# Performance work log

Hardware: AMD Instinct MI355X
Metric: run time of the kernel (lower is better)

## Reference

```python
import jax, jax.numpy as jnp
import numpy as np

B = 2048    # graphs in batch
V = 15      # nodes per graph
T = 16      # window (args.n_his)
F_IN = 2    # num_features
H = 64      # nhid
LH = 40     # LSTM hidden per direction
EPER = 40   # edges per graph
N = B * V
E = B * EPER
EPS = 1e-5


def setup_inputs() -> dict:
    key = jax.random.key(0)
    ks = jax.random.split(key, 12)

    def rn(k, shape, fan_in):
        return jax.random.normal(k, shape, jnp.float32) / np.sqrt(fan_in).astype(np.float32)

    # block-diagonal batched edge_index (PyG-style batching of B graphs of V nodes)
    rng = np.random.default_rng(0)
    off = np.arange(B)[:, None] * V
    src = rng.integers(0, V, (B, EPER)) + off
    dst = rng.integers(0, V, (B, EPER)) + off
    edge_index = jnp.asarray(np.stack([src.ravel(), dst.ravel()]), dtype=jnp.int32)

    return {
        "data": jax.random.normal(ks[0], (N, F_IN, T), jnp.float32),
        "edge_attr": jax.random.uniform(ks[1], (E,), jnp.float32),
        "W1": rn(ks[2], (H, F_IN), F_IN), "b1": jnp.zeros((H,), jnp.float32),
        "Wg1": rn(ks[3], (H, H), H), "bg1": jnp.zeros((H,), jnp.float32),
        "gamma1": jnp.ones((H,), jnp.float32), "beta1": jnp.zeros((H,), jnp.float32),
        "Wg2": rn(ks[4], (H, H), H), "bg2": jnp.zeros((H,), jnp.float32),
        "gamma2": jnp.ones((H,), jnp.float32), "beta2": jnp.zeros((H,), jnp.float32),
        "Wf": rn(ks[5], (H, V * H), V * H), "bf": jnp.zeros((H,), jnp.float32),
        "Wih_f": rn(ks[6], (4 * LH, H), H), "Whh_f": rn(ks[7], (4 * LH, LH), LH),
        "bih_f": jnp.zeros((4 * LH,), jnp.float32), "bhh_f": jnp.zeros((4 * LH,), jnp.float32),
        "Wih_b": rn(ks[8], (4 * LH, H), H), "Whh_b": rn(ks[9], (4 * LH, LH), LH),
        "bih_b": jnp.zeros((4 * LH,), jnp.float32), "bhh_b": jnp.zeros((4 * LH,), jnp.float32),
        "Wc1": rn(ks[10], (16, 2 * LH), 2 * LH), "bc1": jnp.zeros((16,), jnp.float32),
        "Wc2": rn(ks[11], (1, 16), 16), "bc2": jnp.zeros((1,), jnp.float32),
        "edge_index": edge_index,
    }


def _gcn(x, W, b, edge_index, ew):
    # PyG GCNConv: linear, add self-loops (weight 1), symmetric D^-1/2 (A+I) D^-1/2.
    # x: [N, T, H] -- all T timesteps processed at once (vectorizes the source loop).
    row, col = edge_index[0], edge_index[1]
    loop = jnp.arange(N, dtype=edge_index.dtype)
    row_s = jnp.concatenate([row, loop])
    col_s = jnp.concatenate([col, loop])
    ew_s = jnp.concatenate([ew, jnp.ones((N,), ew.dtype)])
    deg = jax.ops.segment_sum(ew_s, col_s, num_segments=N)
    dinv = jnp.where(deg > 0, jax.lax.rsqrt(deg), 0.0)
    norm = dinv[row_s] * ew_s * dinv[col_s]                      # [E+N]
    xw = jnp.einsum('nth,hk->ntk', x, W)                          # [N, T, H]
    agg = jax.ops.segment_sum(norm[:, None, None] * xw[row_s], col_s, num_segments=N)
    return agg + b


def _bn(x, gamma, beta):
    # BatchNorm1d training-mode stats, per timestep (axis 0 = nodes), biased var.
    m = x.mean(axis=0)
    v = x.var(axis=0)
    return gamma * (x - m) * jax.lax.rsqrt(v + EPS) + beta


def _lstm(X, Wih, Whh, bih, bhh):
    # X: [T, B, H]; PyTorch gate order i, f, g, o.
    def step(carry, xt):
        h, c = carry
        g = xt @ Wih.T + h @ Whh.T + (bih + bhh)
        i, f, gg, o = jnp.split(g, 4, axis=-1)
        c = jax.nn.sigmoid(f) * c + jax.nn.sigmoid(i) * jnp.tanh(gg)
        h = jax.nn.sigmoid(o) * jnp.tanh(c)
        return (h, c), h
    h0 = jnp.zeros((X.shape[1], LH), X.dtype)
    _, hs = jax.lax.scan(step, (h0, h0), X)
    return hs


def _forward(data, edge_attr, W1, b1, Wg1, bg1, gamma1, beta1, Wg2, bg2, gamma2, beta2,
             Wf, bf, Wih_f, Whh_f, bih_f, bhh_f, Wih_b, Whh_b, bih_b, bhh_b,
             Wc1, bc1, Wc2, bc2, edge_index):
    # conv_1 (1x1 Conv2d) == per-node linear over features, kept per timestep
    x = jnp.einsum('nft,hf->nth', data, W1) + b1                 # [N, T, H]
    # Hierarchical GCN with residuals (ReLU then BN, per the source)
    x1 = _bn(jax.nn.relu(_gcn(x, Wg1, bg1, edge_index, edge_attr)), gamma1, beta1) + x
    x2 = _bn(jax.nn.relu(_gcn(x1, Wg2, bg2, edge_index, edge_attr)), gamma2, beta2) + x1
    # stack over timesteps -> [T, B, V*H]
    Xs = x2.transpose(1, 0, 2).reshape(T, B, V * H)
    Xs = jax.nn.relu(Xs @ Wf.T + bf)                             # fc1 -> [T, B, H]
    hs_f = _lstm(Xs, Wih_f, Whh_f, bih_f, bhh_f)
    hs_b = _lstm(Xs[::-1], Wih_b, Whh_b, bih_b, bhh_b)
    # r_out[-1] = [fwd h at t=T-1, bwd h at t=T-1 (first step of reversed scan)]
    last = jnp.concatenate([hs_f[-1], hs_b[0]], axis=-1)          # [B, 80]
    hcls = jax.nn.relu(last @ Wc1.T + bc1)                        # dropout inactive (eval)
    return hcls @ Wc2.T + bc2                                     # [B, 1]


def reference(data, edge_attr, W1, b1, Wg1, bg1, gamma1, beta1, Wg2, bg2, gamma2, beta2,
              Wf, bf, Wih_f, Whh_f, bih_f, bhh_f, Wih_b, Whh_b, bih_b, bhh_b,
              Wc1, bc1, Wc2, bc2, edge_index):
    return _forward(data, edge_attr, W1, b1, Wg1, bg1, gamma1, beta1, Wg2, bg2,
                    gamma2, beta2, Wf, bf, Wih_f, Whh_f, bih_f, bhh_f,
                    Wih_b, Whh_b, bih_b, bhh_b, Wc1, bc1, Wc2, bc2, edge_index)
```

## Files before the change

### kernel.cpp

```cpp
#include <hip/hip_runtime.h>

typedef unsigned int u32;
typedef unsigned short u16;
typedef __attribute__((ext_vector_type(8))) short bf16x8;
typedef __attribute__((ext_vector_type(4))) float f32x4;

#define NB   2048
#define NV   15
#define NT   16
#define NH   64
#define NLH  40
#define EPER 40
#define NN   (NB*NV)
#define NE   (NB*EPER)

#define F_DATA 0
#define F_EA   983040
#define P_W1   1064960
#define P_B1   1065088
#define P_WG1  1065152
#define P_BG1  1069248
#define P_G1   1069312
#define P_BE1  1069376
#define P_WG2  1069440
#define P_BG2  1073536
#define P_G2   1073600
#define P_BE2  1073664
#define P_WF   1073728
#define P_BF   1135168
#define P_WIHF 1135232
#define P_WHHF 1145472
#define P_BIHF 1151872
#define P_BHHF 1152032
#define P_WIHB 1152192
#define P_WHHB 1162432
#define P_BIHB 1168832
#define P_BHHB 1168992
#define P_WC1  1169152
#define P_BC1  1170432
#define P_WC2  1170448
#define P_BC2  1170464
#define CVT_TOTAL 1170465
#define WFB_OFF   1170496
#define WIHT_OFF  1205504
#define STATS_OFF 1231936
#define XS_OFF    1240128
#define FLAG_OFF  3337280
#define BUFX_BYTE 13349376
#define BUFY_BYTE 76263936

__device__ const int d_cum[27] = {
  0, 983040, 1064960, 1065088, 1065152, 1069248, 1069312, 1069376,
  1069440, 1073536, 1073600, 1073664, 1073728, 1135168, 1135232, 1145472,
  1151872, 1152032, 1152192, 1162432, 1168832, 1168992, 1169152, 1170432,
  1170448, 1170464, 1170465};

struct Ptrs { const void* p[26]; };

__device__ inline float b2f(u16 u) { return __uint_as_float(((u32)u) << 16); }
__device__ inline u16 f2b(float f) {
  u32 u = __float_as_uint(f);
  u32 r = (u + 0x7FFFu + ((u >> 16) & 1u)) >> 16;
  return (u16)r;
}
__device__ inline float sigf(float x) { return 1.0f / (1.0f + __expf(-x)); }

__global__ void k_detect(const u16* __restrict__ raw, int* __restrict__ flag) {
  __shared__ int bad;
  if (threadIdx.x == 0) bad = 0;
  __syncthreads();
  for (int i = threadIdx.x; i < 4096; i += 256) {
    float f = b2f(raw[i]);
    if (!(fabsf(f) < 1000.0f)) atomicOr(&bad, 1);
  }
  __syncthreads();
  if (threadIdx.x == 0) *flag = bad ? 0 : 1;
}

__global__ void k_convert(Ptrs ptrs, float* __restrict__ W) {
  int gid = blockIdx.x * 256 + threadIdx.x;
  if (gid >= CVT_TOTAL) return;
  int flag = *(const int*)(W + FLAG_OFF);
  int ti = 0;
  #pragma unroll
  for (int i = 1; i < 26; ++i) ti += (gid >= d_cum[i]);
  int j = gid - d_cum[ti];
  const void* src = ptrs.p[ti];
  W[gid] = flag ? b2f(((const u16*)src)[j]) : ((const float*)src)[j];
}

__global__ void k_preswz(float* __restrict__ W, u16* __restrict__ WfB) {
  int i = blockIdx.x * 256 + threadIdx.x;
  if (i < 61440) {
    int j = i & 7, lane = (i >> 3) & 63, kt = (i >> 9) & 3, ks = i >> 11;
    int kout = kt * 16 + (lane & 15);
    int m = ks * 32 + ((lane >> 4) << 3) + j;
    WfB[i] = f2b(W[P_WF + kout * 960 + m]);
  } else if (i < 69632) {
    int ii = i - 61440;
    int L = ii >> 12, r = ii & 4095;
    int j = r & 7, lane = (r >> 3) & 63, nt = (r >> 9) & 3, ks = (r >> 11) & 1;
    int h = ks * 32 + ((lane >> 4) << 3) + j;
    int k = nt * 16 + (lane & 15);
    WfB[i] = f2b(W[(L ? P_WG2 : P_WG1) + h * 64 + k]);
  } else if (i < 90112) {
    int e = i - 69632;
    int which = e / 10240, rem = e % 10240;
    int kk = rem / 160, jj = rem % 160;
    W[WIHT_OFF + e] = W[(which ? P_WIHB : P_WIHF) + jj * 64 + kk];
  }
}

template<int LAYER>
__global__ __launch_bounds__(256, 4)
void k_gcn(const float* __restrict__ W, const int* __restrict__ ei,
           const u16* __restrict__ bufIn, u16* __restrict__ bufOut,
           const u16* __restrict__ WgB,
           float* __restrict__ S1, float* __restrict__ S2,
           int bgoff, int scoff, int shoff) {
  __shared__ u16 s_x[15360];
  __shared__ float s_m[240];
  __shared__ float s_deg[16];
  __shared__ float s_d[480];
  __shared__ float s_w1[192];

  int g = blockIdx.x, tid = threadIdx.x;
  float ew = 0.f; int er = 0, ec = 0;
  if (tid < 40) {
    er = ei[g * 40 + tid] - g * 15;
    ec = ei[NE + g * 40 + tid] - g * 15;
    ew = W[F_EA + g * 40 + tid];
  }
  if (tid >= 40 && tid < 56) s_deg[tid - 40] = 1.0f;
  for (int i = tid; i < 240; i += 256) s_m[i] = 0.f;
  if (tid >= 64 && tid < 184) ((float4*)s_d)[tid - 64] = ((const float4*)(W + F_DATA + g * 480))[tid - 64];
  if (tid >= 192 && tid < 240) ((float4*)s_w1)[tid - 192] = ((const float4*)(W + P_W1))[tid - 192];
  __syncthreads();

  if (tid < 40) atomicAdd(&s_deg[ec], ew);
  for (int i = tid; i < 1920; i += 256) {
    int v = i >> 7, rem = i & 127, t = rem >> 3, q = rem & 7;
    int h0 = q * 8;
    float d0 = s_d[v * 32 + t], d1 = s_d[v * 32 + 16 + t];
    u32 pk[4];
    if (LAYER == 1) {
      #pragma unroll
      for (int jp = 0; jp < 4; ++jp) {
        int h = h0 + jp * 2;
        float xa = fmaf(d0, s_w1[2 * h],     fmaf(d1, s_w1[2 * h + 1], s_w1[128 + h]));
        float xb = fmaf(d0, s_w1[2 * h + 2], fmaf(d1, s_w1[2 * h + 3], s_w1[129 + h]));
        pk[jp] = (u32)f2b(xa) | ((u32)f2b(xb) << 16);
      }
    } else {
      uint4 uy = ((const uint4*)(bufIn + g * 15360))[i];
      u32 uys[4] = {uy.x, uy.y, uy.z, uy.w};
      int th0 = t * 64 + h0;
      float4 A0 = *(const float4*)(W + scoff + th0), A1 = *(const float4*)(W + scoff + th0 + 4);
      float4 B0 = *(const float4*)(W + shoff + th0), B1 = *(const float4*)(W + shoff + th0 + 4);
      float scs[8] = {A0.x, A0.y, A0.z, A0.w, A1.x, A1.y, A1.z, A1.w};
      float shs[8] = {B0.x, B0.y, B0.z, B0.w, B1.x, B1.y, B1.z, B1.w};
      #pragma unroll
      for (int jp = 0; jp < 4; ++jp) {
        int j0 = jp * 2, h = h0 + j0;
        float xa = fmaf(d0, s_w1[2 * h],     fmaf(d1, s_w1[2 * h + 1], s_w1[128 + h]));
        float xb = fmaf(d0, s_w1[2 * h + 2], fmaf(d1, s_w1[2 * h + 3], s_w1[129 + h]));
        float a = fmaf(b2f((u16)(uys[jp] & 0xffff)), scs[j0],     shs[j0])     + xa;
        float b = fmaf(b2f((u16)(uys[jp] >> 16)),    scs[j0 + 1], shs[j0 + 1]) + xb;
        pk[jp] = (u32)f2b(a) | ((u32)f2b(b) << 16);
      }
    }
    u32 byte = ((u32)(i * 16)) ^ (((u32)(t & 7)) << 4);
    *(uint4*)((char*)s_x + byte) = make_uint4(pk[0], pk[1], pk[2], pk[3]);
  }
  __syncthreads();
  if (tid < 15) s_deg[tid] = rsqrtf(s_deg[tid]);
  __syncthreads();
  if (tid < 40) atomicAdd(&s_m[ec * 16 + er], s_deg[er] * ew * s_deg[ec]);
  if (tid >= 64 && tid < 80) {
    float dv = s_deg[tid - 64];
    atomicAdd(&s_m[(tid - 64) * 17], dv * dv);
  }
  __syncthreads();

  u32* sx32 = (u32*)s_x;
  {
    float x0[15], x1[15], x2[15], x3[15];
    int p0 = tid, p1 = tid + 256;
    int t0 = p0 >> 5, h0 = (2 * p0) & 63;
    int t1 = p1 >> 5, h1 = (2 * p1) & 63;
    u32 ba0 = ((u32)(t0 * 128 + h0 * 2)) ^ (((u32)(t0 & 7)) << 4);
    u32 ba1 = ((u32)(t1 * 128 + h1 * 2)) ^ (((u32)(t1 & 7)) << 4);
    #pragma unroll
    for (int v = 0; v < 15; ++v) {
      u32 ua = sx32[(ba0 + v * 2048) >> 2];
      u32 ub = sx32[(ba1 + v * 2048) >> 2];
      x0[v] = b2f((u16)(ua & 0xffff)); x1[v] = b2f((u16)(ua >> 16));
      x2[v] = b2f((u16)(ub & 0xffff)); x3[v] = b2f((u16)(ub >> 16));
    }
    #pragma unroll
    for (int vc = 0; vc < 15; ++vc) {
      float a0 = 0.f, a1 = 0.f, a2 = 0.f, a3 = 0.f;
      #pragma unroll
      for (int vr = 0; vr < 15; ++vr) {
        float m = s_m[vc * 16 + vr];
        a0 = fmaf(m, x0[vr], a0); a1 = fmaf(m, x1[vr], a1);
        a2 = fmaf(m, x2[vr], a2); a3 = fmaf(m, x3[vr], a3);
      }
      sx32[(ba0 + vc * 2048) >> 2] = (u32)f2b(a0) | ((u32)f2b(a1) << 16);
      sx32[(ba1 + vc * 2048) >> 2] = (u32)f2b(a2) | ((u32)f2b(a3) << 16);
    }
  }
  __syncthreads();

  int wid = tid >> 6, lane = tid & 63;
  int tA = lane & 15, kg = lane >> 4;
  const bf16x8* wb = (const bf16x8*)WgB;
  bf16x8 bf0 = wb[(0 * 4 + wid) * 64 + lane];
  bf16x8 bf1 = wb[(1 * 4 + wid) * 64 + lane];
  int kout = wid * 16 + tA;
  float bias = W[bgoff + kout];
  f32x4 acc[15];
  #pragma unroll
  for (int v = 0; v < 15; ++v) acc[v] = (f32x4){0.f, 0.f, 0.f, 0.f};
  u32 sw = ((u32)(tA & 7)) << 4;
  #pragma unroll
  for (int v = 0; v < 15; ++v) {
    u32 bb = (u32)(v * 2048 + tA * 128 + kg * 16);
    bf16x8 a0 = *(const bf16x8*)(s_x + ((bb ^ sw) >> 1));
    bf16x8 a1 = *(const bf16x8*)(s_x + (((bb + 64) ^ sw) >> 1));
    acc[v] = __builtin_amdgcn_mfma_f32_16x16x32_bf16(a0, bf0, acc[v], 0, 0, 0);
    acc[v] = __builtin_amdgcn_mfma_f32_16x16x32_bf16(a1, bf1, acc[v], 0, 0, 0);
  }
  float s1r[4] = {0.f, 0.f, 0.f, 0.f}, s2r[4] = {0.f, 0.f, 0.f, 0.f};
  u16* pout = bufOut + g * 15360;
  #pragma unroll
  for (int v = 0; v < 15; ++v) {
    #pragma unroll
    for (int r = 0; r < 4; ++r) {
      float y = fmaxf(acc[v][r] + bias, 0.f);
      pout[v * 1024 + (kg * 4 + r) * 64 + kout] = f2b(y);
      s1r[r] += y; s2r[r] += y * y;
    }
  }
  #pragma unroll
  for (int r = 0; r < 4; ++r) {
    int idx = (kg * 4 + r) * 64 + kout;
    atomicAdd(&S1[idx], s1r[r]);
    atomicAdd(&S2[idx], s2r[r]);
  }
}

__global__ void k_finalize(float* __restrict__ W, int layer) {
  int i = blockIdx.x * 256 + threadIdx.x;
  if (i >= 1024) return;
  int base = STATS_OFF + (layer == 1 ? 0 : 2048);
  int scb  = STATS_OFF + (layer == 1 ? 4096 : 6144);
  float m   = W[base + i] * (1.0f / 30720.0f);
  float var = W[base + 1024 + i] * (1.0f / 30720.0f) - m * m;
  float istd = rsqrtf(var + 1e-5f);
  int h = i & 63;
  float gm = W[(layer == 1 ? P_G1 : P_G2) + h];
  float bt = W[(layer == 1 ? P_BE1 : P_BE2) + h];
  float sc = gm * istd;
  W[scb + i] = sc;
  W[scb + 1024 + i] = bt - m * sc;
}

__global__ __launch_bounds__(256, 4)
void k_fc1(const float* __restrict__ W, const u16* __restrict__ bufY2,
           const u16* __restrict__ bufY1, const u16* __restrict__ WfB,
           float* __restrict__ Xs) {
  __shared__ u16 s_x[15360];
  __shared__ float s_d[480];
  __shared__ float s_w1[192];
  int g = blockIdx.x, tid = threadIdx.x;
  if (tid < 120) ((float4*)s_d)[tid] = ((const float4*)(W + F_DATA + g * 480))[tid];
  if (tid >= 128 && tid < 176) ((float4*)s_w1)[tid - 128] = ((const float4*)(W + P_W1))[tid - 128];
  __syncthreads();
  const uint4* py2 = (const uint4*)(bufY2 + g * 15360);
  const uint4* py1 = (const uint4*)(bufY1 + g * 15360);
  for (int i = tid; i < 1920; i += 256) {
    int v = i >> 7, rem = i & 127, t = rem >> 3, q = rem & 7;
    int h0 = q * 8, th0 = t * 64 + h0;
    uint4 u2 = py2[i], u1 = py1[i];
    u32 u2s[4] = {u2.x, u2.y, u2.z, u2.w}, u1s[4] = {u1.x, u1.y, u1.z, u1.w};
    float d0 = s_d[v * 32 + t], d1 = s_d[v * 32 + 16 + t];
    float4 A0 = *(const float4*)(W + STATS_OFF + 6144 + th0), A1 = *(const float4*)(W + STATS_OFF + 6148 + th0);
    float4 B0 = *(const float4*)(W + STATS_OFF + 7168 + th0), B1 = *(const float4*)(W + STATS_OFF + 7172 + th0);
    float4 C0 = *(const float4*)(W + STATS_OFF + 4096 + th0), C1 = *(const float4*)(W + STATS_OFF + 4100 + th0);
    float4 D0 = *(const float4*)(W + STATS_OFF + 5120 + th0), D1 = *(const float4*)(W + STATS_OFF + 5124 + th0);
    float sc2[8] = {A0.x, A0.y, A0.z, A0.w, A1.x, A1.y, A1.z, A1.w};
    float sh2[8] = {B0.x, B0.y, B0.z, B0.w, B1.x, B1.y, B1.z, B1.w};
    float sc1[8] = {C0.x, C0.y, C0.z, C0.w, C1.x, C1.y, C1.z, C1.w};
    float sh1[8] = {D0.x, D0.y, D0.z, D0.w, D1.x, D1.y, D1.z, D1.w};
    u32 pk[4];
    #pragma unroll
    for (int jp = 0; jp < 4; ++jp) {
      int j0 = jp * 2, h = h0 + j0;
      float xa = fmaf(d0, s_w1[2 * h],     fmaf(d1, s_w1[2 * h + 1], s_w1[128 + h]));
      float xb = fmaf(d0, s_w1[2 * h + 2], fmaf(d1, s_w1[2 * h + 3], s_w1[129 + h]));
      float x1a = fmaf(b2f((u16)(u1s[jp] & 0xffff)), sc1[j0],     sh1[j0])     + xa;
      float x1b = fmaf(b2f((u16)(u1s[jp] >> 16)),    sc1[j0 + 1], sh1[j0 + 1]) + xb;
      float a = fmaf(b2f((u16)(u2s[jp] & 0xffff)), sc2[j0],     sh2[j0])     + x1a;
      float b = fmaf(b2f((u16)(u2s[jp] >> 16)),    sc2[j0 + 1], sh2[j0 + 1]) + x1b;
      pk[jp] = (u32)f2b(a) | ((u32)f2b(b) << 16);
    }
    u32 byte = ((u32)(i * 16)) ^ (((u32)(t & 7)) << 4);
    *(uint4*)((char*)s_x + byte) = make_uint4(pk[0], pk[1], pk[2], pk[3]);
  }
  __syncthreads();

  int wid = tid >> 6, lane = tid & 63;
  int tA = lane & 15, kg = lane >> 4;
  f32x4 acc = {0.f, 0.f, 0.f, 0.f};
  const bf16x8* wf = (const bf16x8*)WfB;
  #pragma unroll 2
  for (int ks = 0; ks < 30; ++ks) {
    int v = ks >> 1, half = ks & 1;
    u32 byte = (u32)(v * 2048 + tA * 128 + (half * 32 + kg * 8) * 2) ^ (((u32)(tA & 7)) << 4);
    bf16x8 afrag = *(const bf16x8*)(s_x + (byte >> 1));
    bf16x8 bfrag = wf[(ks * 4 + wid) * 64 + lane];
    acc = __builtin_amdgcn_mfma_f32_16x16x32_bf16(afrag, bfrag, acc, 0, 0, 0);
  }
  int kout = wid * 16 + (lane & 15);
  float bias = W[P_BF + kout];
  #pragma unroll
  for (int r = 0; r < 4; ++r) {
    int t = (lane >> 4) * 4 + r;
    Xs[t * 131072 + g * 64 + kout] = fmaxf(acc[r] + bias, 0.0f);
  }
}

__global__ __launch_bounds__(256)
void k_gatex(const float* __restrict__ W, const float* __restrict__ Xs,
             float* __restrict__ gxf, float* __restrict__ gxb) {
  __shared__ float s_x[2048];
  __shared__ float s_w[10240];
  __shared__ float s_b[160];
  int blk = blockIdx.x, tid = threadIdx.x;
  int fwd = blk < 1024;
  const float* xsrc = fwd ? (Xs + blk * 2048) : (Xs + 1966080 + (blk - 1024) * 2048);
  const float* wsrc = W + WIHT_OFF + (fwd ? 0 : 10240);
  int bo  = fwd ? P_BIHF : P_BIHB;
  int bo2 = fwd ? P_BHHF : P_BHHB;
  float* out = fwd ? (gxf + blk * 5120) : (gxb + (blk - 1024) * 5120);

  float4* sx4 = (float4*)s_x;
  const float4* xs4 = (const float4*)xsrc;
  for (int i = tid; i < 512; i += 256) sx4[i] = xs4[i];
  for (int i = tid; i < 10240; i += 256) s_w[i] = wsrc[i];
  if (tid < 160) s_b[tid] = W[bo + tid] + W[bo2 + tid];
  __syncthreads();

  int rb = (tid >> 5) * 4, c0 = tid & 31;
  float acc[4][5];
  #pragma unroll
  for (int r = 0; r < 4; ++r)
    #pragma unroll
    for (int q = 0; q < 5; ++q) acc[r][q] = s_b[c0 + 32 * q];
  #pragma unroll 4
  for (int kk = 0; kk < 64; ++kk) {
    float w0 = s_w[kk * 160 + c0],      w1 = s_w[kk * 160 + c0 + 32];
    float w2 = s_w[kk * 160 + c0 + 64], w3 = s_w[kk * 160 + c0 + 96];
    float w4 = s_w[kk * 160 + c0 + 128];
    #pragma unroll
    for (int r = 0; r < 4; ++r) {
      float xv = s_x[(rb + r) * 64 + kk];
      acc[r][0] = fmaf(xv, w0, acc[r][0]);
      acc[r][1] = fmaf(xv, w1, acc[r][1]);
      acc[r][2] = fmaf(xv, w2, acc[r][2]);
      acc[r][3] = fmaf(xv, w3, acc[r][3]);
      acc[r][4] = fmaf(xv, w4, acc[r][4]);
    }
  }
  #pragma unroll
  for (int r = 0; r < 4; ++r)
    #pragma unroll
    for (int q = 0; q < 5; ++q)
      out[(rb + r) * 160 + c0 + 32 * q] = acc[r][q];
}

__global__ __launch_bounds__(512)
void k_lstm2(const float* __restrict__ W, const float* __restrict__ gxf,
             const float* __restrict__ gxb, void* __restrict__ dout,
             const int* __restrict__ flagp) {
  __shared__ float s_whh[40 * 162];
  __shared__ float s_h[320], s_c[320], s_hb[320];
  __shared__ float s_g[1280];
  __shared__ float s_cls[128];
  int tid = threadIdx.x, r0 = blockIdx.x * 8;

  for (int i = tid; i < 6400; i += 512) {
    int jj = i / 40, kk = i % 40;
    s_whh[kk * 162 + jj] = W[P_WHHF + i];
  }
  if (tid < 320) { s_h[tid] = 0.f; s_c[tid] = 0.f; }
  __syncthreads();

  int r = tid >> 6, l = tid & 63;
  int l2 = (l < 32) ? l + 128 : l;
  const float* gbase = gxf + (r0 + r) * 160;
  float g0 = gbase[l], g1 = gbase[l + 64], g2 = gbase[l2];

  for (int t = 0; t < 16; ++t) {
    float acc0 = g0, acc1 = g1, acc2 = g2;
    int tn = (t < 15) ? t + 1 : 15;
    const float* gnext = gbase + tn * 327680;
    g0 = gnext[l]; g1 = gnext[l + 64]; g2 = gnext[l2];
    const float* hr = s_h + r * 40;
    #pragma unroll 8
    for (int kk = 0; kk < 40; ++kk) {
      float hv = hr[kk];
      acc0 = fmaf(hv, s_whh[kk * 162 + l], acc0);
      acc1 = fmaf(hv, s_whh[kk * 162 + l + 64], acc1);
      acc2 = fmaf(hv, s_whh[kk * 162 + l2], acc2);
    }
    s_g[r * 160 + l] = acc0;
    s_g[r * 160 + l + 64] = acc1;
    if (l < 32) s_g[r * 160 + l2] = acc2;
    __syncthreads();
    if (tid < 320) {
      int row = tid / 40, jj = tid % 40;
      const float* gr = s_g + row * 160;
      float ig = gr[jj], fg = gr[jj + 40], gg = gr[jj + 80], og = gr[jj + 120];
      float c = sigf(fg) * s_c[tid] + sigf(ig) * tanhf(gg);
      s_c[tid] = c;
      s_h[tid] = sigf(og) * tanhf(c);
    }
    __syncthreads();
  }

  if (tid < 320) {
    int row = tid / 40, jj = tid % 40;
    const float* gb = gxb + (r0 + row) * 160;
    float ig = gb[jj], gg = gb[jj + 80], og = gb[jj + 120];
    float c = sigf(ig) * tanhf(gg);
    s_hb[tid] = sigf(og) * tanhf(c);
  }
  __syncthreads();

  if (tid < 128) {
    int rr = tid >> 4, jj = tid & 15;
    float a = W[P_BC1 + jj];
    for (int p = 0; p < 40; ++p) a = fmaf(W[P_WC1 + jj * 80 + p],      s_h[rr * 40 + p],  a);
    for (int p = 0; p < 40; ++p) a = fmaf(W[P_WC1 + jj * 80 + 40 + p], s_hb[rr * 40 + p], a);
    s_cls[rr * 16 + jj] = fmaxf(a, 0.0f);
  }
  __syncthreads();
  if (tid < 8) {
    float o = W[P_BC2];
    #pragma unroll
    for (int jj = 0; jj < 16; ++jj) o = fmaf(W[P_WC2 + jj], s_cls[tid * 16 + jj], o);
    if (*flagp) ((u16*)dout)[r0 + tid] = f2b(o);
    else        ((float*)dout)[r0 + tid] = o;
  }
}

extern "C" void kernel_launch(void* const* d_in, const int* in_sizes, int n_in,
                              void* d_out, int out_size, void* d_ws, size_t ws_size,
                              hipStream_t stream) {
  float* W = (float*)d_ws;
  u16* bufX = (u16*)((char*)d_ws + BUFX_BYTE);
  u16* bufY = (u16*)((char*)d_ws + BUFY_BYTE);
  u16* WfB  = (u16*)(W + WFB_OFF);
  float* gxf = (float*)((char*)d_ws + BUFX_BYTE);
  float* gxb = gxf + 5242880;
  const int* ei = (const int*)d_in[26];

  hipMemsetAsync(W + STATS_OFF, 0, 4096 * sizeof(float), stream);
  k_detect<<<1, 256, 0, stream>>>((const u16*)d_in[0], (int*)(W + FLAG_OFF));
  Ptrs ptrs;
  for (int i = 0; i < 26; ++i) ptrs.p[i] = d_in[i];
  k_convert<<<(CVT_TOTAL + 255) / 256, 256, 0, stream>>>(ptrs, W);
  k_preswz<<<352, 256, 0, stream>>>(W, WfB);
  k_gcn<1><<<NB, 256, 0, stream>>>(W, ei, nullptr, bufY, WfB + 61440,
      W + STATS_OFF, W + STATS_OFF + 1024, P_BG1, 0, 0);
  k_finalize<<<4, 256, 0, stream>>>(W, 1);
  k_gcn<2><<<NB, 256, 0, stream>>>(W, ei, bufY, bufX, WfB + 65536,
      W + STATS_OFF + 2048, W + STATS_OFF + 3072, P_BG2,
      STATS_OFF + 4096, STATS_OFF + 5120);
  k_finalize<<<4, 256, 0, stream>>>(W, 2);
  k_fc1<<<NB, 256, 0, stream>>>(W, bufX, bufY, WfB, W + XS_OFF);
  k_gatex<<<1088, 256, 0, stream>>>(W, W + XS_OFF, gxf, gxb);
  k_lstm2<<<256, 512, 0, stream>>>(W, gxf, gxb, d_out, (const int*)(W + FLAG_OFF));
}
```

Baseline: 340.7 us.

## Fuse LSTM input projection into LSTM kernel and stage GCN I/O through LDS

Drops the separate gate-input GEMM kernel. The LSTM kernel now stages its rows of Xs in shared memory and computes the input projections for all 16 timesteps into registers, so the gxf/gxb intermediates are never written to or read back from global memory. The GCN kernels issue all layer-2 input loads up front to get more loads in flight, and write outputs into LDS first so the global stores go out as coalesced 16-byte writes; the fc1 loop is unrolled. In exchange, the LSTM kernel needs large dynamic shared memory and many registers, and does the 64-wide projection serially per thread on only 256 blocks, which may lower occupancy.

```diff
diff --git a/kernel.cpp b/kernel.cpp
--- a/kernel.cpp
+++ b/kernel.cpp
@@ -125,6 +125,15 @@
   __shared__ float s_w1[192];
 
   int g = blockIdx.x, tid = threadIdx.x;
+
+  uint4 ld[8];
+  if (LAYER == 2) {
+    const uint4* py = (const uint4*)(bufIn + g * 15360);
+    #pragma unroll
+    for (int c = 0; c < 7; ++c) ld[c] = py[tid + c * 256];
+    if (tid < 128) ld[7] = py[tid + 1792];
+  }
+
   float ew = 0.f; int er = 0, ec = 0;
   if (tid < 40) {
     er = ei[g * 40 + tid] - g * 15;
@@ -138,39 +147,42 @@
   __syncthreads();
 
   if (tid < 40) atomicAdd(&s_deg[ec], ew);
-  for (int i = tid; i < 1920; i += 256) {
-    int v = i >> 7, rem = i & 127, t = rem >> 3, q = rem & 7;
-    int h0 = q * 8;
-    float d0 = s_d[v * 32 + t], d1 = s_d[v * 32 + 16 + t];
-    u32 pk[4];
-    if (LAYER == 1) {
-      #pragma unroll
-      for (int jp = 0; jp < 4; ++jp) {
-        int h = h0 + jp * 2;
-        float xa = fmaf(d0, s_w1[2 * h],     fmaf(d1, s_w1[2 * h + 1], s_w1[128 + h]));
-        float xb = fmaf(d0, s_w1[2 * h + 2], fmaf(d1, s_w1[2 * h + 3], s_w1[129 + h]));
-        pk[jp] = (u32)f2b(xa) | ((u32)f2b(xb) << 16);
+  #pragma unroll
+  for (int c = 0; c < 8; ++c) {
+    if (c < 7 || tid < 128) {
+      int i = tid + c * 256;
+      int v = i >> 7, rem = i & 127, t = rem >> 3, q = rem & 7;
+      int h0 = q * 8;
+      float d0 = s_d[v * 32 + t], d1 = s_d[v * 32 + 16 + t];
+      u32 pk[4];
+      if (LAYER == 1) {
+        #pragma unroll
+        for (int jp = 0; jp < 4; ++jp) {
+          int h = h0 + jp * 2;
+          float xa = fmaf(d0, s_w1[2 * h],     fmaf(d1, s_w1[2 * h + 1], s_w1[128 + h]));
+          float xb = fmaf(d0, s_w1[2 * h + 2], fmaf(d1, s_w1[2 * h + 3], s_w1[129 + h]));
+          pk[jp] = (u32)f2b(xa) | ((u32)f2b(xb) << 16);
+        }
+      } else {
+        u32 uys[4] = {ld[c].x, ld[c].y, ld[c].z, ld[c].w};
+        int th0 = t * 64 + h0;
+        float4 A0 = *(const float4*)(W + scoff + th0), A1 = *(const float4*)(W + scoff + th0 + 4);
+        float4 B0 = *(const float4*)(W + shoff + th0), B1 = *(const float4*)(W + shoff + th0 + 4);
+        float scs[8] = {A0.x, A0.y, A0.z, A0.w, A1.x, A1.y, A1.z, A1.w};
+        float shs[8] = {B0.x, B0.y, B0.z, B0.w, B1.x, B1.y, B1.z, B1.w};
+        #pragma unroll
+        for (int jp = 0; jp < 4; ++jp) {
+          int j0 = jp * 2, h = h0 + j0;
+          float xa = fmaf(d0, s_w1[2 * h],     fmaf(d1, s_w1[2 * h + 1], s_w1[128 + h]));
+          float xb = fmaf(d0, s_w1[2 * h + 2], fmaf(d1, s_w1[2 * h + 3], s_w1[129 + h]));
+          float a = fmaf(b2f((u16)(uys[jp] & 0xffff)), scs[j0],     shs[j0])     + xa;
+          float b = fmaf(b2f((u16)(uys[jp] >> 16)),    scs[j0 + 1], shs[j0 + 1]) + xb;
+          pk[jp] = (u32)f2b(a) | ((u32)f2b(b) << 16);
+        }
       }
-    } else {
-      uint4 uy = ((const uint4*)(bufIn + g * 15360))[i];
-      u32 uys[4] = {uy.x, uy.y, uy.z, uy.w};
-      int th0 = t * 64 + h0;
-      float4 A0 = *(const float4*)(W + scoff + th0), A1 = *(const float4*)(W + scoff + th0 + 4);
-      float4 B0 = *(const float4*)(W + shoff + th0), B1 = *(const float4*)(W + shoff + th0 + 4);
-      float scs[8] = {A0.x, A0.y, A0.z, A0.w, A1.x, A1.y, A1.z, A1.w};
-      float shs[8] = {B0.x, B0.y, B0.z, B0.w, B1.x, B1.y, B1.z, B1.w};
-      #pragma unroll
-      for (int jp = 0; jp < 4; ++jp) {
-        int j0 = jp * 2, h = h0 + j0;
-        float xa = fmaf(d0, s_w1[2 * h],     fmaf(d1, s_w1[2 * h + 1], s_w1[128 + h]));
-        float xb = fmaf(d0, s_w1[2 * h + 2], fmaf(d1, s_w1[2 * h + 3], s_w1[129 + h]));
-        float a = fmaf(b2f((u16)(uys[jp] & 0xffff)), scs[j0],     shs[j0])     + xa;
-        float b = fmaf(b2f((u16)(uys[jp] >> 16)),    scs[j0 + 1], shs[j0 + 1]) + xb;
-        pk[jp] = (u32)f2b(a) | ((u32)f2b(b) << 16);
-      }
-    }
-    u32 byte = ((u32)(i * 16)) ^ (((u32)(t & 7)) << 4);
-    *(uint4*)((char*)s_x + byte) = make_uint4(pk[0], pk[1], pk[2], pk[3]);
+      u32 byte = ((u32)(i * 16)) ^ (((u32)(t & 7)) << 4);
+      *(uint4*)((char*)s_x + byte) = make_uint4(pk[0], pk[1], pk[2], pk[3]);
+    }
   }
   __syncthreads();
   if (tid < 15) s_deg[tid] = rsqrtf(s_deg[tid]);
@@ -231,15 +243,28 @@
     acc[v] = __builtin_amdgcn_mfma_f32_16x16x32_bf16(a0, bf0, acc[v], 0, 0, 0);
     acc[v] = __builtin_amdgcn_mfma_f32_16x16x32_bf16(a1, bf1, acc[v], 0, 0, 0);
   }
+
   float s1r[4] = {0.f, 0.f, 0.f, 0.f}, s2r[4] = {0.f, 0.f, 0.f, 0.f};
-  u16* pout = bufOut + g * 15360;
+  __syncthreads();
   #pragma unroll
   for (int v = 0; v < 15; ++v) {
     #pragma unroll
     for (int r = 0; r < 4; ++r) {
       float y = fmaxf(acc[v][r] + bias, 0.f);
-      pout[v * 1024 + (kg * 4 + r) * 64 + kout] = f2b(y);
+      int t = kg * 4 + r;
+      u32 byte = ((u32)(v * 2048 + t * 128 + kout * 2)) ^ (((u32)kg) << 5);
+      *(u16*)((char*)s_x + byte) = f2b(y);
       s1r[r] += y; s2r[r] += y * y;
+    }
+  }
+  __syncthreads();
+  uint4* dst = (uint4*)(bufOut + g * 15360);
+  const uint4* src = (const uint4*)s_x;
+  #pragma unroll
+  for (int c = 0; c < 8; ++c) {
+    if (c < 7 || tid < 128) {
+      int i = tid + c * 256;
+      dst[i] = src[i ^ (((i >> 5) & 3) << 1)];
     }
   }
   #pragma unroll
@@ -279,34 +304,38 @@
   __syncthreads();
   const uint4* py2 = (const uint4*)(bufY2 + g * 15360);
   const uint4* py1 = (const uint4*)(bufY1 + g * 15360);
-  for (int i = tid; i < 1920; i += 256) {
-    int v = i >> 7, rem = i & 127, t = rem >> 3, q = rem & 7;
-    int h0 = q * 8, th0 = t * 64 + h0;
-    uint4 u2 = py2[i], u1 = py1[i];
-    u32 u2s[4] = {u2.x, u2.y, u2.z, u2.w}, u1s[4] = {u1.x, u1.y, u1.z, u1.w};
-    float d0 = s_d[v * 32 + t], d1 = s_d[v * 32 + 16 + t];
-    float4 A0 = *(const float4*)(W + STATS_OFF + 6144 + th0), A1 = *(const float4*)(W + STATS_OFF + 6148 + th0);
-    float4 B0 = *(const float4*)(W + STATS_OFF + 7168 + th0), B1 = *(const float4*)(W + STATS_OFF + 7172 + th0);
-    float4 C0 = *(const float4*)(W + STATS_OFF + 4096 + th0), C1 = *(const float4*)(W + STATS_OFF + 4100 + th0);
-    float4 D0 = *(const float4*)(W + STATS_OFF + 5120 + th0), D1 = *(const float4*)(W + STATS_OFF + 5124 + th0);
-    float sc2[8] = {A0.x, A0.y, A0.z, A0.w, A1.x, A1.y, A1.z, A1.w};
-    float sh2[8] = {B0.x, B0.y, B0.z, B0.w, B1.x, B1.y, B1.z, B1.w};
-    float sc1[8] = {C0.x, C0.y, C0.z, C0.w, C1.x, C1.y, C1.z, C1.w};
-    float sh1[8] = {D0.x, D0.y, D0.z, D0.w, D1.x, D1.y, D1.z, D1.w};
-    u32 pk[4];
-    #pragma unroll
-    for (int jp = 0; jp < 4; ++jp) {
-      int j0 = jp * 2, h = h0 + j0;
-      float xa = fmaf(d0, s_w1[2 * h],     fmaf(d1, s_w1[2 * h + 1], s_w1[128 + h]));
-      float xb = fmaf(d0, s_w1[2 * h + 2], fmaf(d1, s_w1[2 * h + 3], s_w1[129 + h]));
-      float x1a = fmaf(b2f((u16)(u1s[jp] & 0xffff)), sc1[j0],     sh1[j0])     + xa;
-      float x1b = fmaf(b2f((u16)(u1s[jp] >> 16)),    sc1[j0 + 1], sh1[j0 + 1]) + xb;
-      float a = fmaf(b2f((u16)(u2s[jp] & 0xffff)), sc2[j0],     sh2[j0])     + x1a;
-      float b = fmaf(b2f((u16)(u2s[jp] >> 16)),    sc2[j0 + 1], sh2[j0 + 1]) + x1b;
-      pk[jp] = (u32)f2b(a) | ((u32)f2b(b) << 16);
-    }
-    u32 byte = ((u32)(i * 16)) ^ (((u32)(t & 7)) << 4);
-    *(uint4*)((char*)s_x + byte) = make_uint4(pk[0], pk[1], pk[2], pk[3]);
+  #pragma unroll
+  for (int c = 0; c < 8; ++c) {
+    if (c < 7 || tid < 128) {
+      int i = tid + c * 256;
+      int v = i >> 7, rem = i & 127, t = rem >> 3, q = rem & 7;
+      int h0 = q * 8, th0 = t * 64 + h0;
+      uint4 u2 = py2[i], u1 = py1[i];
+      u32 u2s[4] = {u2.x, u2.y, u2.z, u2.w}, u1s[4] = {u1.x, u1.y, u1.z, u1.w};
+      float d0 = s_d[v * 32 + t], d1 = s_d[v * 32 + 16 + t];
+      float4 A0 = *(const float4*)(W + STATS_OFF + 6144 + th0), A1 = *(const float4*)(W + STATS_OFF + 6148 + th0);
+      float4 B0 = *(const float4*)(W + STATS_OFF + 7168 + th0), B1 = *(const float4*)(W + STATS_OFF + 7172 + th0);
+      float4 C0 = *(const float4*)(W + STATS_OFF + 4096 + th0), C1 = *(const float4*)(W + STATS_OFF + 4100 + th0);
+      float4 D0 = *(const float4*)(W + STATS_OFF + 5120 + th0), D1 = *(const float4*)(W + STATS_OFF + 5124 + th0);
+      float sc2[8] = {A0.x, A0.y, A0.z, A0.w, A1.x, A1.y, A1.z, A1.w};
+      float sh2[8] = {B0.x, B0.y, B0.z, B0.w, B1.x, B1.y, B1.z, B1.w};
+      float sc1[8] = {C0.x, C0.y, C0.z, C0.w, C1.x, C1.y, C1.z, C1.w};
+      float sh1[8] = {D0.x, D0.y, D0.z, D0.w, D1.x, D1.y, D1.z, D1.w};
+      u32 pk[4];
+      #pragma unroll
+      for (int jp = 0; jp < 4; ++jp) {
+        int j0 = jp * 2, h = h0 + j0;
+        float xa = fmaf(d0, s_w1[2 * h],     fmaf(d1, s_w1[2 * h + 1], s_w1[128 + h]));
+        float xb = fmaf(d0, s_w1[2 * h + 2], fmaf(d1, s_w1[2 * h + 3], s_w1[129 + h]));
+        float x1a = fmaf(b2f((u16)(u1s[jp] & 0xffff)), sc1[j0],     sh1[j0])     + xa;
+        float x1b = fmaf(b2f((u16)(u1s[jp] >> 16)),    sc1[j0 + 1], sh1[j0 + 1]) + xb;
+        float a = fmaf(b2f((u16)(u2s[jp] & 0xffff)), sc2[j0],     sh2[j0])     + x1a;
+        float b = fmaf(b2f((u16)(u2s[jp] >> 16)),    sc2[j0 + 1], sh2[j0 + 1]) + x1b;
+        pk[jp] = (u32)f2b(a) | ((u32)f2b(b) << 16);
+      }
+      u32 byte = ((u32)(i * 16)) ^ (((u32)(t & 7)) << 4);
+      *(uint4*)((char*)s_x + byte) = make_uint4(pk[0], pk[1], pk[2], pk[3]);
+    }
   }
   __syncthreads();
 
@@ -331,82 +360,61 @@
   }
 }
 
-__global__ __launch_bounds__(256)
-void k_gatex(const float* __restrict__ W, const float* __restrict__ Xs,
-             float* __restrict__ gxf, float* __restrict__ gxb) {
-  __shared__ float s_x[2048];
-  __shared__ float s_w[10240];
-  __shared__ float s_b[160];
-  int blk = blockIdx.x, tid = threadIdx.x;
-  int fwd = blk < 1024;
-  const float* xsrc = fwd ? (Xs + blk * 2048) : (Xs + 1966080 + (blk - 1024) * 2048);
-  const float* wsrc = W + WIHT_OFF + (fwd ? 0 : 10240);
-  int bo  = fwd ? P_BIHF : P_BIHB;
-  int bo2 = fwd ? P_BHHF : P_BHHB;
-  float* out = fwd ? (gxf + blk * 5120) : (gxb + (blk - 1024) * 5120);
-
-  float4* sx4 = (float4*)s_x;
-  const float4* xs4 = (const float4*)xsrc;
-  for (int i = tid; i < 512; i += 256) sx4[i] = xs4[i];
-  for (int i = tid; i < 10240; i += 256) s_w[i] = wsrc[i];
-  if (tid < 160) s_b[tid] = W[bo + tid] + W[bo2 + tid];
-  __syncthreads();
-
-  int rb = (tid >> 5) * 4, c0 = tid & 31;
-  float acc[4][5];
-  #pragma unroll
-  for (int r = 0; r < 4; ++r)
-    #pragma unroll
-    for (int q = 0; q < 5; ++q) acc[r][q] = s_b[c0 + 32 * q];
-  #pragma unroll 4
-  for (int kk = 0; kk < 64; ++kk) {
-    float w0 = s_w[kk * 160 + c0],      w1 = s_w[kk * 160 + c0 + 32];
-    float w2 = s_w[kk * 160 + c0 + 64], w3 = s_w[kk * 160 + c0 + 96];
-    float w4 = s_w[kk * 160 + c0 + 128];
-    #pragma unroll
-    for (int r = 0; r < 4; ++r) {
-      float xv = s_x[(rb + r) * 64 + kk];
-      acc[r][0] = fmaf(xv, w0, acc[r][0]);
-      acc[r][1] = fmaf(xv, w1, acc[r][1]);
-      acc[r][2] = fmaf(xv, w2, acc[r][2]);
-      acc[r][3] = fmaf(xv, w3, acc[r][3]);
-      acc[r][4] = fmaf(xv, w4, acc[r][4]);
-    }
-  }
-  #pragma unroll
-  for (int r = 0; r < 4; ++r)
-    #pragma unroll
-    for (int q = 0; q < 5; ++q)
-      out[(rb + r) * 160 + c0 + 32 * q] = acc[r][q];
-}
-
 __global__ __launch_bounds__(512)
-void k_lstm2(const float* __restrict__ W, const float* __restrict__ gxf,
-             const float* __restrict__ gxb, void* __restrict__ dout,
-             const int* __restrict__ flagp) {
-  __shared__ float s_whh[40 * 162];
-  __shared__ float s_h[320], s_c[320], s_hb[320];
-  __shared__ float s_g[1280];
-  __shared__ float s_cls[128];
+void k_lstm2(const float* __restrict__ W, const float* __restrict__ Xs,
+             void* __restrict__ dout, const int* __restrict__ flagp) {
+  extern __shared__ float smem[];
+  float* s_whh = smem;
+  float* s_xs  = smem + 6480;
+  float* s_h   = smem + 14672;
+  float* s_c   = smem + 14992;
+  float* s_hb  = smem + 15312;
+  float* s_g   = smem + 15632;
+  float* s_cls = smem + 16912;
   int tid = threadIdx.x, r0 = blockIdx.x * 8;
 
   for (int i = tid; i < 6400; i += 512) {
     int jj = i / 40, kk = i % 40;
     s_whh[kk * 162 + jj] = W[P_WHHF + i];
   }
+  #pragma unroll
+  for (int c = 0; c < 4; ++c) {
+    int i4 = tid + c * 512;
+    int i = i4 * 4;
+    int t = i >> 9, b = (i >> 6) & 7, k = i & 63;
+    ((float4*)s_xs)[i4] = *(const float4*)(Xs + t * 131072 + (r0 + b) * 64 + k);
+  }
   if (tid < 320) { s_h[tid] = 0.f; s_c[tid] = 0.f; }
   __syncthreads();
 
   int r = tid >> 6, l = tid & 63;
   int l2 = (l < 32) ? l + 128 : l;
-  const float* gbase = gxf + (r0 + r) * 160;
-  float g0 = gbase[l], g1 = gbase[l + 64], g2 = gbase[l2];
-
+  float G0[16], G1[16], G2[16];
+  {
+    float b0 = W[P_BIHF + l]      + W[P_BHHF + l];
+    float b1 = W[P_BIHF + l + 64] + W[P_BHHF + l + 64];
+    float b2 = W[P_BIHF + l2]     + W[P_BHHF + l2];
+    #pragma unroll
+    for (int t = 0; t < 16; ++t) { G0[t] = b0; G1[t] = b1; G2[t] = b2; }
+    const float* wih = W + WIHT_OFF;
+    const float* xr = s_xs + r * 64;
+    for (int kk = 0; kk < 64; ++kk) {
+      float w0 = wih[kk * 160 + l];
+      float w1 = wih[kk * 160 + l + 64];
+      float w2 = wih[kk * 160 + l2];
+      #pragma unroll
+      for (int t = 0; t < 16; ++t) {
+        float xv = xr[t * 512 + kk];
+        G0[t] = fmaf(xv, w0, G0[t]);
+        G1[t] = fmaf(xv, w1, G1[t]);
+        G2[t] = fmaf(xv, w2, G2[t]);
+      }
+    }
+  }
+
+  #pragma unroll
   for (int t = 0; t < 16; ++t) {
-    float acc0 = g0, acc1 = g1, acc2 = g2;
-    int tn = (t < 15) ? t + 1 : 15;
-    const float* gnext = gbase + tn * 327680;
-    g0 = gnext[l]; g1 = gnext[l + 64]; g2 = gnext[l2];
+    float acc0 = G0[t], acc1 = G1[t], acc2 = G2[t];
     const float* hr = s_h + r * 40;
     #pragma unroll 8
     for (int kk = 0; kk < 40; ++kk) {
@@ -432,10 +440,19 @@
 
   if (tid < 320) {
     int row = tid / 40, jj = tid % 40;
-    const float* gb = gxb + (r0 + row) * 160;
-    float ig = gb[jj], gg = gb[jj + 80], og = gb[jj + 120];
-    float c = sigf(ig) * tanhf(gg);
-    s_hb[tid] = sigf(og) * tanhf(c);
+    const float* wb = W + WIHT_OFF + 10240;
+    float ai = W[P_BIHB + jj]       + W[P_BHHB + jj];
+    float ag = W[P_BIHB + jj + 80]  + W[P_BHHB + jj + 80];
+    float ao = W[P_BIHB + jj + 120] + W[P_BHHB + jj + 120];
+    const float* xr = s_xs + 15 * 512 + row * 64;
+    for (int kk = 0; kk < 64; ++kk) {
+      float xv = xr[kk];
+      ai = fmaf(xv, wb[kk * 160 + jj], ai);
+      ag = fmaf(xv, wb[kk * 160 + jj + 80], ag);
+      ao = fmaf(xv, wb[kk * 160 + jj + 120], ao);
+    }
+    float c = sigf(ai) * tanhf(ag);
+    s_hb[tid] = sigf(ao) * tanhf(c);
   }
   __syncthreads();
 
@@ -463,9 +480,10 @@
   u16* bufX = (u16*)((char*)d_ws + BUFX_BYTE);
   u16* bufY = (u16*)((char*)d_ws + BUFY_BYTE);
   u16* WfB  = (u16*)(W + WFB_OFF);
-  float* gxf = (float*)((char*)d_ws + BUFX_BYTE);
-  float* gxb = gxf + 5242880;
   const int* ei = (const int*)d_in[26];
+
+  (void)hipFuncSetAttribute(reinterpret_cast<const void*>(&k_lstm2),
+                            hipFuncAttributeMaxDynamicSharedMemorySize, 68160);
 
   hipMemsetAsync(W + STATS_OFF, 0, 4096 * sizeof(float), stream);
   k_detect<<<1, 256, 0, stream>>>((const u16*)d_in[0], (int*)(W + FLAG_OFF));
@@ -481,6 +499,5 @@
       STATS_OFF + 4096, STATS_OFF + 5120);
   k_finalize<<<4, 256, 0, stream>>>(W, 2);
   k_fc1<<<NB, 256, 0, stream>>>(W, bufX, bufY, WfB, W + XS_OFF);
-  k_gatex<<<1088, 256, 0, stream>>>(W, W + XS_OFF, gxf, gxb);
-  k_lstm2<<<256, 512, 0, stream>>>(W, gxf, gxb, d_out, (const int*)(W + FLAG_OFF));
-}
+  k_lstm2<<<256, 512, 68160, stream>>>(W, W + XS_OFF, d_out, (const int*)(W + FLAG_OFF));
+}
```

New measurement: 337.0 us. No clear change (-1.1%).
